# Optimization experiments

Measured on AMD Instinct MI355X. Metric: run time of the kernel, lower is better.

Reference implementation:

```python
import jax, jax.numpy as jnp
import numpy as np

B, T, ENC, DEC, U = 64, 2048, 512, 512, 128

def setup_inputs() -> dict:
    key = jax.random.key(0)
    ks = jax.random.split(key, 8)
    s_dec = 1.0 / np.sqrt(DEC)
    s_enc = 1.0 / np.sqrt(ENC)
    s_u = 1.0 / np.sqrt(U)
    return {
        "decoder_hidden": jax.random.normal(ks[0], (B, DEC), jnp.float32),
        "encoder_outputs": jax.random.normal(ks[1], (B, T, ENC), jnp.float32),
        "Wa": jax.random.normal(ks[2], (DEC, U), jnp.float32) * s_dec,
        "ba": jnp.zeros((U,), jnp.float32),
        "Wb": jax.random.normal(ks[3], (ENC, U), jnp.float32) * s_enc,
        "bb": jnp.zeros((U,), jnp.float32),
        "Wv": jax.random.normal(ks[4], (U, 1), jnp.float32) * s_u,
        "bv": jnp.zeros((1,), jnp.float32),
    }

def reference(decoder_hidden, encoder_outputs, Wa, ba, Wb, bb, Wv, bv):
    # q: [B, 1, U] — decoder hidden projected, broadcast over time
    q = (decoder_hidden @ Wa + ba)[:, None, :]
    # k: [B, T, U]
    k = jnp.einsum('bte,eu->btu', encoder_outputs, Wb) + bb
    # score: [B, T, 1]
    score = jnp.tanh(q + k) @ Wv + bv
    attn = jax.nn.softmax(score, axis=1)          # [B, T, 1]
    context = jnp.sum(attn * encoder_outputs, axis=1)  # [B, ENC]
    return context, attn
```

## Files before the change

kernel.cpp:

```cpp
#include <hip/hip_runtime.h>
#include <math.h>

#define B_   64
#define T_   2048
#define ENC_ 512
#define U_   128
#define NC   16
#define MBLK 128

typedef __attribute__((ext_vector_type(8))) _Float16 half8;
typedef __attribute__((ext_vector_type(4))) float float4v;

__device__ __forceinline__ void async_ld16(const void* g, void* l) {
    __builtin_amdgcn_global_load_lds(
        (const __attribute__((address_space(1))) void*)g,
        (__attribute__((address_space(3))) void*)l, 16, 0, 0);
}

__device__ inline void cvt_split8_f16(const float4 a0, const float4 a1,
                                      half8& h, half8& l) {
    const float xs[8] = {a0.x, a0.y, a0.z, a0.w, a1.x, a1.y, a1.z, a1.w};
#pragma unroll
    for (int j = 0; j < 8; ++j) {
        const _Float16 hi = (_Float16)xs[j];
        h[j] = hi;
        l[j] = (_Float16)(xs[j] - (float)hi);
    }
}

__device__ inline float fast_tanh(float x) {
    const float e = __expf(2.0f * x);
    return 1.0f - 2.0f / (e + 1.0f);
}

__global__ __launch_bounds__(256)
void prep_kernel(const float* __restrict__ dh,
                 const float* __restrict__ Wa,
                 const float* __restrict__ ba,
                 const float* __restrict__ bb,
                 const float* __restrict__ Wb,
                 float* __restrict__ q,
                 _Float16* __restrict__ whf,
                 float* __restrict__ uz) {
    const int blk = blockIdx.x;
    const int tid = threadIdx.x;
    if (blk < 64) {
        if (tid < U_) {
            const int b = blk, u = tid;
            const float* dhb = dh + b * ENC_;
            float a0 = 0.f, a1 = 0.f, a2 = 0.f, a3 = 0.f;
#pragma unroll 4
            for (int e = 0; e < ENC_; e += 4) {
                a0 += dhb[e + 0] * Wa[(e + 0) * U_ + u];
                a1 += dhb[e + 1] * Wa[(e + 1) * U_ + u];
                a2 += dhb[e + 2] * Wa[(e + 2) * U_ + u];
                a3 += dhb[e + 3] * Wa[(e + 3) * U_ + u];
            }
            q[b * U_ + u] = ((a0 + a1) + (a2 + a3)) + ba[u] + bb[u];
        }
    } else if (blk < 96) {
        const int fid = (blk - 64) * 4 + (tid >> 6);
        const int c   = fid >> 3;
        const int gn  = fid & 7;
        const int L   = tid & 63;
        const int n   = gn * 16 + (L & 15);
        const int k0  = c * 32 + (L >> 4) * 8;
        half8 hi;
#pragma unroll
        for (int j = 0; j < 8; ++j)
            hi[j] = (_Float16)Wb[(size_t)(k0 + j) * U_ + n];
        *(half8*)(whf + ((size_t)fid * 64 + L) * 8) = hi;
    } else {
        const int i = (blk - 96) * 256 + tid;
        if (i < B_ * ENC_ + B_) uz[i] = 0.f;
    }
}

__global__ __launch_bounds__(256, 3)
void score_ctx_kernel(const float* __restrict__ enc,
                      const _Float16* __restrict__ whf,
                      const float* __restrict__ q,
                      const float* __restrict__ Wv,
                      float* __restrict__ expw,
                      float* __restrict__ uctx,
                      float* __restrict__ Zsum) {
    __shared__ __align__(16) float    As[2][4096];
    __shared__ __align__(16) _Float16 Bs[2][4096];
    __shared__ float ew[MBLK];

    const int tid = threadIdx.x;
    const int w   = tid >> 6;
    const int L   = tid & 63;
    const int m0  = blockIdx.x * MBLK;
    const int b   = m0 >> 11;

    const int arow = w * 32 + (L >> 3);
    const int akf  = ((L & 7) ^ (L >> 3)) * 4;
    const float* aprow = enc + (size_t)(m0 + arow) * ENC_ + akf;
    const _Float16* bprow = whf + w * 1024 + L * 8;

    float4v acc[2][8];
#pragma unroll
    for (int mi = 0; mi < 2; ++mi)
#pragma unroll
        for (int gi = 0; gi < 8; ++gi) acc[mi][gi] = (float4v)0.f;

    {
#pragma unroll
        for (int j = 0; j < 4; ++j)
            async_ld16(aprow + (size_t)j * 8 * ENC_, &As[0][w * 1024 + j * 256]);
#pragma unroll
        for (int j = 0; j < 2; ++j)
            async_ld16(bprow + j * 512, &Bs[0][w * 1024 + j * 512]);
    }
    __syncthreads();

    for (int c = 0; c < NC; ++c) {
        const int cur = c & 1;

        if (c < NC - 1) {
            const int nxt = cur ^ 1;
            const float* ap = aprow + (c + 1) * 32;
#pragma unroll
            for (int j = 0; j < 4; ++j)
                async_ld16(ap + (size_t)j * 8 * ENC_, &As[nxt][w * 1024 + j * 256]);
            const _Float16* bp = bprow + (size_t)(c + 1) * 4096;
#pragma unroll
            for (int j = 0; j < 2; ++j)
                async_ld16(bp + j * 512, &Bs[nxt][w * 1024 + j * 512]);
        }

        half8 bh[8];
#pragma unroll
        for (int gi = 0; gi < 8; ++gi)
            bh[gi] = *(const half8*)(&Bs[cur][(gi * 64 + L) * 8]);

        half8 ah[2], al[2];
#pragma unroll
        for (int mi = 0; mi < 2; ++mi) {
            const int row = w * 32 + mi * 16 + (L & 15);
            const int s4  = (row & 7) * 4;
            const int k0  = (L >> 4) * 8;
            const float4 x0 = *(const float4*)(&As[cur][row * 32 + (k0 ^ s4)]);
            const float4 x1 = *(const float4*)(&As[cur][row * 32 + ((k0 + 4) ^ s4)]);
            cvt_split8_f16(x0, x1, ah[mi], al[mi]);
        }

#pragma unroll
        for (int mi = 0; mi < 2; ++mi)
#pragma unroll
            for (int gi = 0; gi < 8; ++gi) {
                acc[mi][gi] = __builtin_amdgcn_mfma_f32_16x16x32_f16(ah[mi], bh[gi], acc[mi][gi], 0, 0, 0);
                acc[mi][gi] = __builtin_amdgcn_mfma_f32_16x16x32_f16(al[mi], bh[gi], acc[mi][gi], 0, 0, 0);
            }

        __syncthreads();
    }

    const int n15 = L & 15;
    float qv[8], wvv[8];
#pragma unroll
    for (int gi = 0; gi < 8; ++gi) {
        const int u = gi * 16 + n15;
        qv[gi]  = q[b * U_ + u];
        wvv[gi] = Wv[u];
    }
#pragma unroll
    for (int mi = 0; mi < 2; ++mi) {
#pragma unroll
        for (int r = 0; r < 4; ++r) {
            float s = 0.f;
#pragma unroll
            for (int gi = 0; gi < 8; ++gi)
                s += fast_tanh(qv[gi] + acc[mi][gi][r]) * wvv[gi];
            s += __shfl_xor(s, 1, 64);
            s += __shfl_xor(s, 2, 64);
            s += __shfl_xor(s, 4, 64);
            s += __shfl_xor(s, 8, 64);
            if (n15 == 0) {
                const int mrow = w * 32 + mi * 16 + (L >> 4) * 4 + r;
                const float e = __expf(s);
                ew[mrow] = e;
                expw[m0 + mrow] = e;
            }
        }
    }
    __syncthreads();

    const int col = tid * 2;
    const float* ebase = enc + (size_t)m0 * ENC_ + col;
    float sx = 0.f, sy = 0.f;
#pragma unroll 8
    for (int t = 0; t < MBLK; ++t) {
        const float wgt = ew[t];
        const float2 v = *(const float2*)(ebase + (size_t)t * ENC_);
        sx += wgt * v.x;
        sy += wgt * v.y;
    }
    atomicAdd(&uctx[b * ENC_ + col], sx);
    atomicAdd(&uctx[b * ENC_ + col + 1], sy);

    if (tid < 64) {
        float z = ew[tid] + ew[tid + 64];
        z += __shfl_xor(z, 1, 64);
        z += __shfl_xor(z, 2, 64);
        z += __shfl_xor(z, 4, 64);
        z += __shfl_xor(z, 8, 64);
        z += __shfl_xor(z, 16, 64);
        z += __shfl_xor(z, 32, 64);
        if (tid == 0) atomicAdd(&Zsum[b], z);
    }
}

__global__ void normalize_kernel(const float* __restrict__ uctx,
                                 const float* __restrict__ Zsum,
                                 const float* __restrict__ expw,
                                 float* __restrict__ ctx,
                                 float* __restrict__ attn) {
    const int idx = blockIdx.x * 256 + threadIdx.x;
    if (idx < B_ * ENC_) {
        ctx[idx] = uctx[idx] / Zsum[idx >> 9];
    } else {
        const int i2 = idx - B_ * ENC_;
        attn[i2] = expw[i2] / Zsum[i2 >> 11];
    }
}

extern "C" void kernel_launch(void* const* d_in, const int* in_sizes, int n_in,
                              void* d_out, int out_size, void* d_ws, size_t ws_size,
                              hipStream_t stream) {
    const float* dh  = (const float*)d_in[0];
    const float* enc = (const float*)d_in[1];
    const float* Wa  = (const float*)d_in[2];
    const float* ba  = (const float*)d_in[3];
    const float* Wb  = (const float*)d_in[4];
    const float* bb  = (const float*)d_in[5];
    const float* Wv  = (const float*)d_in[6];

    float* out      = (float*)d_out;
    float* ctx      = out;
    float* attn_out = out + (B_ * ENC_);

    float* ws   = (float*)d_ws;
    float* q    = ws;
    float* expw = ws + 8192;
    float* uctx = ws + 8192 + B_ * T_;
    float* Zs   = uctx + B_ * ENC_;
    _Float16* whf = (_Float16*)(Zs + 64);

    prep_kernel<<<225, 256, 0, stream>>>(dh, Wa, ba, bb, Wb, q, whf, uctx);
    score_ctx_kernel<<<(B_ * T_) / MBLK, 256, 0, stream>>>(enc, whf, q, Wv,
                                                           expw, uctx, Zs);
    normalize_kernel<<<(B_ * (ENC_ + T_)) / 256, 256, 0, stream>>>(uctx, Zs, expw,
                                                                   ctx, attn_out);
}
```

Baseline: 437.8 us.

## Load Wb fragments directly to registers and replace block barriers with per-wave waitcnts

Wb fragments are now read straight from global memory into registers each chunk instead of being staged through LDS, which removes the Bs shared buffer. Each wave loads and consumes only its own rows of the A tile, so the per-iteration __syncthreads is replaced by manual s_waitcnt vmcnt/lgkmcnt counters, with the last chunk peeled out of the loop. The aim is to cut barrier stalls and LDS traffic and to lower LDS use per block. The risk is that the hand-set vmcnt values must exactly match the number of outstanding loads the compiler issues, and global B loads add L2 traffic and latency to every chunk.

```diff
diff --git a/kernel.cpp b/kernel.cpp
--- a/kernel.cpp
+++ b/kernel.cpp
@@ -84,8 +84,7 @@
                       float* __restrict__ expw,
                       float* __restrict__ uctx,
                       float* __restrict__ Zsum) {
-    __shared__ __align__(16) float    As[2][4096];
-    __shared__ __align__(16) _Float16 Bs[2][4096];
+    __shared__ __align__(16) float As[2][4096];
     __shared__ float ew[MBLK];
 
     const int tid = threadIdx.x;
@@ -97,7 +96,6 @@
     const int arow = w * 32 + (L >> 3);
     const int akf  = ((L & 7) ^ (L >> 3)) * 4;
     const float* aprow = enc + (size_t)(m0 + arow) * ENC_ + akf;
-    const _Float16* bprow = whf + w * 1024 + L * 8;
 
     float4v acc[2][8];
 #pragma unroll
@@ -105,35 +103,27 @@
 #pragma unroll
         for (int gi = 0; gi < 8; ++gi) acc[mi][gi] = (float4v)0.f;
 
-    {
+#pragma unroll
+    for (int j = 0; j < 4; ++j)
+        async_ld16(aprow + (size_t)j * 8 * ENC_, &As[0][w * 1024 + j * 256]);
+
+    for (int c = 0; c < NC - 1; ++c) {
+        const int cur = c & 1;
+        const int nxt = cur ^ 1;
+
+        half8 bh[8];
+        const _Float16* bp = whf + (size_t)c * 4096 + L * 8;
+#pragma unroll
+        for (int gi = 0; gi < 8; ++gi)
+            bh[gi] = *(const half8*)(bp + gi * 512);
+
+        asm volatile("s_waitcnt lgkmcnt(0)" ::: "memory");
+        const float* ap = aprow + (c + 1) * 32;
 #pragma unroll
         for (int j = 0; j < 4; ++j)
-            async_ld16(aprow + (size_t)j * 8 * ENC_, &As[0][w * 1024 + j * 256]);
-#pragma unroll
-        for (int j = 0; j < 2; ++j)
-            async_ld16(bprow + j * 512, &Bs[0][w * 1024 + j * 512]);
-    }
-    __syncthreads();
-
-    for (int c = 0; c < NC; ++c) {
-        const int cur = c & 1;
-
-        if (c < NC - 1) {
-            const int nxt = cur ^ 1;
-            const float* ap = aprow + (c + 1) * 32;
-#pragma unroll
-            for (int j = 0; j < 4; ++j)
-                async_ld16(ap + (size_t)j * 8 * ENC_, &As[nxt][w * 1024 + j * 256]);
-            const _Float16* bp = bprow + (size_t)(c + 1) * 4096;
-#pragma unroll
-            for (int j = 0; j < 2; ++j)
-                async_ld16(bp + j * 512, &Bs[nxt][w * 1024 + j * 512]);
-        }
-
-        half8 bh[8];
-#pragma unroll
-        for (int gi = 0; gi < 8; ++gi)
-            bh[gi] = *(const half8*)(&Bs[cur][(gi * 64 + L) * 8]);
+            async_ld16(ap + (size_t)j * 8 * ENC_, &As[nxt][w * 1024 + j * 256]);
+
+        asm volatile("s_waitcnt vmcnt(12)" ::: "memory");
 
         half8 ah[2], al[2];
 #pragma unroll
@@ -153,8 +143,36 @@
                 acc[mi][gi] = __builtin_amdgcn_mfma_f32_16x16x32_f16(ah[mi], bh[gi], acc[mi][gi], 0, 0, 0);
                 acc[mi][gi] = __builtin_amdgcn_mfma_f32_16x16x32_f16(al[mi], bh[gi], acc[mi][gi], 0, 0, 0);
             }
-
-        __syncthreads();
+    }
+
+    {
+        const int c   = NC - 1;
+        const int cur = c & 1;
+        half8 bh[8];
+        const _Float16* bp = whf + (size_t)c * 4096 + L * 8;
+#pragma unroll
+        for (int gi = 0; gi < 8; ++gi)
+            bh[gi] = *(const half8*)(bp + gi * 512);
+
+        asm volatile("s_waitcnt vmcnt(8)" ::: "memory");
+
+        half8 ah[2], al[2];
+#pragma unroll
+        for (int mi = 0; mi < 2; ++mi) {
+            const int row = w * 32 + mi * 16 + (L & 15);
+            const int s4  = (row & 7) * 4;
+            const int k0  = (L >> 4) * 8;
+            const float4 x0 = *(const float4*)(&As[cur][row * 32 + (k0 ^ s4)]);
+            const float4 x1 = *(const float4*)(&As[cur][row * 32 + ((k0 + 4) ^ s4)]);
+            cvt_split8_f16(x0, x1, ah[mi], al[mi]);
+        }
+#pragma unroll
+        for (int mi = 0; mi < 2; ++mi)
+#pragma unroll
+            for (int gi = 0; gi < 8; ++gi) {
+                acc[mi][gi] = __builtin_amdgcn_mfma_f32_16x16x32_f16(ah[mi], bh[gi], acc[mi][gi], 0, 0, 0);
+                acc[mi][gi] = __builtin_amdgcn_mfma_f32_16x16x32_f16(al[mi], bh[gi], acc[mi][gi], 0, 0, 0);
+            }
     }
 
     const int n15 = L & 15;
```

Result: no change. 431.1 us (-1.5%).

## Remove block barriers with per-wave 4-stage A pipeline and register-prefetched B

Applied to the files above, without the earlier changes.

Each wave now loads only its own A rows into a 4-deep LDS ring and waits with explicit vmcnt/lgkmcnt counts, so the per-chunk __syncthreads is dropped. The fp16 B fragments are prefetched straight from global memory into registers one chunk ahead instead of staged through shared memory. The LDS layout gains padding (GSTRIDE) and a new swizzle. This adds register pressure, so the occupancy hint drops from 3 to 2 blocks, and correctness depends on the hand-counted waitcnt values matching the issued loads.

```diff
diff --git a/kernel.cpp b/kernel.cpp
--- a/kernel.cpp
+++ b/kernel.cpp
@@ -7,6 +7,7 @@
 #define U_   128
 #define NC   16
 #define MBLK 128
+#define GSTRIDE 264
 
 typedef __attribute__((ext_vector_type(8))) _Float16 half8;
 typedef __attribute__((ext_vector_type(4))) float float4v;
@@ -76,7 +77,7 @@
     }
 }
 
-__global__ __launch_bounds__(256, 3)
+__global__ __launch_bounds__(256, 2)
 void score_ctx_kernel(const float* __restrict__ enc,
                       const _Float16* __restrict__ whf,
                       const float* __restrict__ q,
@@ -84,8 +85,7 @@
                       float* __restrict__ expw,
                       float* __restrict__ uctx,
                       float* __restrict__ Zsum) {
-    __shared__ __align__(16) float    As[2][4096];
-    __shared__ __align__(16) _Float16 Bs[2][4096];
+    __shared__ __align__(16) float As[4][16 * GSTRIDE];
     __shared__ float ew[MBLK];
 
     const int tid = threadIdx.x;
@@ -97,7 +97,6 @@
     const int arow = w * 32 + (L >> 3);
     const int akf  = ((L & 7) ^ (L >> 3)) * 4;
     const float* aprow = enc + (size_t)(m0 + arow) * ENC_ + akf;
-    const _Float16* bprow = whf + w * 1024 + L * 8;
 
     float4v acc[2][8];
 #pragma unroll
@@ -105,44 +104,53 @@
 #pragma unroll
         for (int gi = 0; gi < 8; ++gi) acc[mi][gi] = (float4v)0.f;
 
+#pragma unroll
+    for (int j = 0; j < 4; ++j)
+        async_ld16(aprow + (size_t)j * 8 * ENC_, &As[0][(w * 4 + j) * GSTRIDE]);
+#pragma unroll
+    for (int j = 0; j < 4; ++j)
+        async_ld16(aprow + 32 + (size_t)j * 8 * ENC_, &As[1][(w * 4 + j) * GSTRIDE]);
+    half8 pb[8];
     {
-#pragma unroll
-        for (int j = 0; j < 4; ++j)
-            async_ld16(aprow + (size_t)j * 8 * ENC_, &As[0][w * 1024 + j * 256]);
-#pragma unroll
-        for (int j = 0; j < 2; ++j)
-            async_ld16(bprow + j * 512, &Bs[0][w * 1024 + j * 512]);
-    }
-    __syncthreads();
-
+        const _Float16* bp = whf + L * 8;
+#pragma unroll
+        for (int gi = 0; gi < 8; ++gi) pb[gi] = *(const half8*)(bp + gi * 512);
+    }
+
+#pragma unroll
     for (int c = 0; c < NC; ++c) {
-        const int cur = c & 1;
-
-        if (c < NC - 1) {
-            const int nxt = cur ^ 1;
-            const float* ap = aprow + (c + 1) * 32;
+        half8 bh[8];
+#pragma unroll
+        for (int gi = 0; gi < 8; ++gi) bh[gi] = pb[gi];
+
+        if (c + 1 < NC) {
+            const _Float16* bp = whf + (size_t)(c + 1) * 4096 + L * 8;
+#pragma unroll
+            for (int gi = 0; gi < 8; ++gi) pb[gi] = *(const half8*)(bp + gi * 512);
+        }
+
+        if (c + 2 < NC) {
+            asm volatile("s_waitcnt lgkmcnt(0)" ::: "memory");
+            const float* ap = aprow + (c + 2) * 32;
 #pragma unroll
             for (int j = 0; j < 4; ++j)
-                async_ld16(ap + (size_t)j * 8 * ENC_, &As[nxt][w * 1024 + j * 256]);
-            const _Float16* bp = bprow + (size_t)(c + 1) * 4096;
-#pragma unroll
-            for (int j = 0; j < 2; ++j)
-                async_ld16(bp + j * 512, &Bs[nxt][w * 1024 + j * 512]);
-        }
-
-        half8 bh[8];
-#pragma unroll
-        for (int gi = 0; gi < 8; ++gi)
-            bh[gi] = *(const half8*)(&Bs[cur][(gi * 64 + L) * 8]);
-
+                async_ld16(ap + (size_t)j * 8 * ENC_,
+                           &As[(c + 2) & 3][(w * 4 + j) * GSTRIDE]);
+        }
+
+        if (c < NC - 2)       asm volatile("s_waitcnt vmcnt(24)" ::: "memory");
+        else if (c == NC - 2) asm volatile("s_waitcnt vmcnt(20)" ::: "memory");
+        else                  asm volatile("s_waitcnt vmcnt(8)"  ::: "memory");
+
+        const float* Ab = &As[c & 3][0];
         half8 ah[2], al[2];
 #pragma unroll
         for (int mi = 0; mi < 2; ++mi) {
-            const int row = w * 32 + mi * 16 + (L & 15);
-            const int s4  = (row & 7) * 4;
-            const int k0  = (L >> 4) * 8;
-            const float4 x0 = *(const float4*)(&As[cur][row * 32 + (k0 ^ s4)]);
-            const float4 x1 = *(const float4*)(&As[cur][row * 32 + ((k0 + 4) ^ s4)]);
+            const int g  = w * 4 + mi * 2 + ((L >> 3) & 1);
+            const int rr = L & 7;
+            const int kg = (L >> 4) * 2;
+            const float4 x0 = *(const float4*)(Ab + g * GSTRIDE + rr * 32 + ((kg ^ rr) * 4));
+            const float4 x1 = *(const float4*)(Ab + g * GSTRIDE + rr * 32 + (((kg + 1) ^ rr) * 4));
             cvt_split8_f16(x0, x1, ah[mi], al[mi]);
         }
 
@@ -153,8 +161,6 @@
                 acc[mi][gi] = __builtin_amdgcn_mfma_f32_16x16x32_f16(ah[mi], bh[gi], acc[mi][gi], 0, 0, 0);
                 acc[mi][gi] = __builtin_amdgcn_mfma_f32_16x16x32_f16(al[mi], bh[gi], acc[mi][gi], 0, 0, 0);
             }
-
-        __syncthreads();
     }
 
     const int n15 = L & 15;
```

New measurement: 427.5 us. 2.4% less time.

## Stage whole encoder tile as split-f16 in LDS and reuse it for context

Applied to the files above, without the earlier changes.

The block tile shrinks to 32 rows. The whole 32x512 encoder slab is loaded once, split into hi/lo f16 and stored in swizzled LDS. The Wb fragments now stream from global memory straight into registers through a 3-deep register prefetch, and four waves split the N dimension in two, with partial scores combined through shared memory. The context sum reads the LDS copy instead of reloading encoder rows from global memory, which removes the second global pass over the encoder. The cost is 4x more blocks and atomics, 64KB of LDS per block (occupancy hint lowered to 2), and a context computed from the hi+lo f16 reconstruction.

```diff
diff --git a/kernel.cpp b/kernel.cpp
--- a/kernel.cpp
+++ b/kernel.cpp
@@ -6,22 +6,16 @@
 #define ENC_ 512
 #define U_   128
 #define NC   16
-#define MBLK 128
+#define MBLK 32
 
 typedef __attribute__((ext_vector_type(8))) _Float16 half8;
+typedef __attribute__((ext_vector_type(4))) _Float16 half4;
 typedef __attribute__((ext_vector_type(4))) float float4v;
 
-__device__ __forceinline__ void async_ld16(const void* g, void* l) {
-    __builtin_amdgcn_global_load_lds(
-        (const __attribute__((address_space(1))) void*)g,
-        (__attribute__((address_space(3))) void*)l, 16, 0, 0);
-}
-
-__device__ inline void cvt_split8_f16(const float4 a0, const float4 a1,
-                                      half8& h, half8& l) {
-    const float xs[8] = {a0.x, a0.y, a0.z, a0.w, a1.x, a1.y, a1.z, a1.w};
-#pragma unroll
-    for (int j = 0; j < 8; ++j) {
+__device__ inline void cvt_split4(const float4 a, half4& h, half4& l) {
+    const float xs[4] = {a.x, a.y, a.z, a.w};
+#pragma unroll
+    for (int j = 0; j < 4; ++j) {
         const _Float16 hi = (_Float16)xs[j];
         h[j] = hi;
         l[j] = (_Float16)(xs[j] - (float)hi);
@@ -76,7 +70,7 @@
     }
 }
 
-__global__ __launch_bounds__(256, 3)
+__global__ __launch_bounds__(256, 2)
 void score_ctx_kernel(const float* __restrict__ enc,
                       const _Float16* __restrict__ whf,
                       const float* __restrict__ q,
@@ -84,8 +78,9 @@
                       float* __restrict__ expw,
                       float* __restrict__ uctx,
                       float* __restrict__ Zsum) {
-    __shared__ __align__(16) float    As[2][4096];
-    __shared__ __align__(16) _Float16 Bs[2][4096];
+    __shared__ __align__(16) _Float16 Ah[MBLK * ENC_];
+    __shared__ __align__(16) _Float16 Al[MBLK * ENC_];
+    __shared__ float sred[2 * MBLK];
     __shared__ float ew[MBLK];
 
     const int tid = threadIdx.x;
@@ -94,120 +89,128 @@
     const int m0  = blockIdx.x * MBLK;
     const int b   = m0 >> 11;
 
-    const int arow = w * 32 + (L >> 3);
-    const int akf  = ((L & 7) ^ (L >> 3)) * 4;
-    const float* aprow = enc + (size_t)(m0 + arow) * ENC_ + akf;
-    const _Float16* bprow = whf + w * 1024 + L * 8;
-
-    float4v acc[2][8];
-#pragma unroll
-    for (int mi = 0; mi < 2; ++mi)
-#pragma unroll
-        for (int gi = 0; gi < 8; ++gi) acc[mi][gi] = (float4v)0.f;
-
     {
-#pragma unroll
-        for (int j = 0; j < 4; ++j)
-            async_ld16(aprow + (size_t)j * 8 * ENC_, &As[0][w * 1024 + j * 256]);
-#pragma unroll
-        for (int j = 0; j < 2; ++j)
-            async_ld16(bprow + j * 512, &Bs[0][w * 1024 + j * 512]);
+        const int l = L;
+        const int g = w;
+        float4 xa[8], xb[8];
+#pragma unroll
+        for (int j = 0; j < 8; ++j) {
+            const float* rp = enc + (size_t)(m0 + j * 4 + g) * ENC_;
+            xa[j] = *(const float4*)(rp + l * 4);
+            xb[j] = *(const float4*)(rp + 256 + l * 4);
+        }
+#pragma unroll
+        for (int j = 0; j < 8; ++j) {
+            const int row = j * 4 + g;
+            const int rs  = row & 7;
+            const int rb  = row * ENC_;
+            {
+                half4 h, lo; cvt_split4(xa[j], h, lo);
+                const int off = rb + (((l >> 1) ^ rs) * 8) + (l & 1) * 4;
+                *(half4*)(Ah + off) = h;  *(half4*)(Al + off) = lo;
+            }
+            {
+                half4 h, lo; cvt_split4(xb[j], h, lo);
+                const int off = rb + ((((l >> 1) + 32) ^ rs) * 8) + (l & 1) * 4;
+                *(half4*)(Ah + off) = h;  *(half4*)(Al + off) = lo;
+            }
+        }
     }
     __syncthreads();
 
+    const int wr  = w >> 1;
+    const int wc  = w & 1;
+    const int n15 = L & 15;
+    const int aq  = L >> 4;
+    const int arow  = wr * 16 + n15;
+    const int abase = arow * ENC_;
+    const int ars   = arow & 7;
+
+    float4v acc[4];
+#pragma unroll
+    for (int gi = 0; gi < 4; ++gi) acc[gi] = (float4v)0.f;
+
+    half8 pb[3][4];
+#pragma unroll
+    for (int gi = 0; gi < 4; ++gi) {
+        pb[0][gi] = *(const half8*)(whf + ((size_t)((0 * 8 + wc * 4 + gi) * 64 + L)) * 8);
+        pb[1][gi] = *(const half8*)(whf + ((size_t)((1 * 8 + wc * 4 + gi) * 64 + L)) * 8);
+    }
+
+#pragma unroll
     for (int c = 0; c < NC; ++c) {
-        const int cur = c & 1;
-
-        if (c < NC - 1) {
-            const int nxt = cur ^ 1;
-            const float* ap = aprow + (c + 1) * 32;
-#pragma unroll
-            for (int j = 0; j < 4; ++j)
-                async_ld16(ap + (size_t)j * 8 * ENC_, &As[nxt][w * 1024 + j * 256]);
-            const _Float16* bp = bprow + (size_t)(c + 1) * 4096;
-#pragma unroll
-            for (int j = 0; j < 2; ++j)
-                async_ld16(bp + j * 512, &Bs[nxt][w * 1024 + j * 512]);
-        }
-
-        half8 bh[8];
-#pragma unroll
-        for (int gi = 0; gi < 8; ++gi)
-            bh[gi] = *(const half8*)(&Bs[cur][(gi * 64 + L) * 8]);
-
-        half8 ah[2], al[2];
-#pragma unroll
-        for (int mi = 0; mi < 2; ++mi) {
-            const int row = w * 32 + mi * 16 + (L & 15);
-            const int s4  = (row & 7) * 4;
-            const int k0  = (L >> 4) * 8;
-            const float4 x0 = *(const float4*)(&As[cur][row * 32 + (k0 ^ s4)]);
-            const float4 x1 = *(const float4*)(&As[cur][row * 32 + ((k0 + 4) ^ s4)]);
-            cvt_split8_f16(x0, x1, ah[mi], al[mi]);
-        }
-
-#pragma unroll
-        for (int mi = 0; mi < 2; ++mi)
-#pragma unroll
-            for (int gi = 0; gi < 8; ++gi) {
-                acc[mi][gi] = __builtin_amdgcn_mfma_f32_16x16x32_f16(ah[mi], bh[gi], acc[mi][gi], 0, 0, 0);
-                acc[mi][gi] = __builtin_amdgcn_mfma_f32_16x16x32_f16(al[mi], bh[gi], acc[mi][gi], 0, 0, 0);
-            }
-
-        __syncthreads();
-    }
-
-    const int n15 = L & 15;
-    float qv[8], wvv[8];
-#pragma unroll
-    for (int gi = 0; gi < 8; ++gi) {
-        const int u = gi * 16 + n15;
+        if (c + 2 < NC) {
+#pragma unroll
+            for (int gi = 0; gi < 4; ++gi)
+                pb[(c + 2) % 3][gi] = *(const half8*)(whf +
+                    ((size_t)(((c + 2) * 8 + wc * 4 + gi) * 64 + L)) * 8);
+        }
+        const int slot = (c * 4 + aq) ^ ars;
+        const half8 ah = *(const half8*)(Ah + abase + slot * 8);
+        const half8 al = *(const half8*)(Al + abase + slot * 8);
+#pragma unroll
+        for (int gi = 0; gi < 4; ++gi) {
+            acc[gi] = __builtin_amdgcn_mfma_f32_16x16x32_f16(ah, pb[c % 3][gi], acc[gi], 0, 0, 0);
+            acc[gi] = __builtin_amdgcn_mfma_f32_16x16x32_f16(al, pb[c % 3][gi], acc[gi], 0, 0, 0);
+        }
+    }
+
+    float qv[4], wvv[4];
+#pragma unroll
+    for (int gi = 0; gi < 4; ++gi) {
+        const int u = wc * 64 + gi * 16 + n15;
         qv[gi]  = q[b * U_ + u];
         wvv[gi] = Wv[u];
     }
 #pragma unroll
-    for (int mi = 0; mi < 2; ++mi) {
-#pragma unroll
-        for (int r = 0; r < 4; ++r) {
-            float s = 0.f;
-#pragma unroll
-            for (int gi = 0; gi < 8; ++gi)
-                s += fast_tanh(qv[gi] + acc[mi][gi][r]) * wvv[gi];
-            s += __shfl_xor(s, 1, 64);
-            s += __shfl_xor(s, 2, 64);
-            s += __shfl_xor(s, 4, 64);
-            s += __shfl_xor(s, 8, 64);
-            if (n15 == 0) {
-                const int mrow = w * 32 + mi * 16 + (L >> 4) * 4 + r;
-                const float e = __expf(s);
-                ew[mrow] = e;
-                expw[m0 + mrow] = e;
-            }
+    for (int r = 0; r < 4; ++r) {
+        float s = 0.f;
+#pragma unroll
+        for (int gi = 0; gi < 4; ++gi)
+            s += fast_tanh(qv[gi] + acc[gi][r]) * wvv[gi];
+        s += __shfl_xor(s, 1, 64);
+        s += __shfl_xor(s, 2, 64);
+        s += __shfl_xor(s, 4, 64);
+        s += __shfl_xor(s, 8, 64);
+        if (n15 == 0) {
+            const int brow = wr * 16 + (L >> 4) * 4 + r;
+            sred[wc * MBLK + brow] = s;
         }
     }
     __syncthreads();
 
-    const int col = tid * 2;
-    const float* ebase = enc + (size_t)m0 * ENC_ + col;
+    if (tid < MBLK) {
+        const float s = sred[tid] + sred[MBLK + tid];
+        const float e = __expf(s);
+        ew[tid] = e;
+        expw[m0 + tid] = e;
+    }
+    __syncthreads();
+
+    typedef __attribute__((ext_vector_type(2))) _Float16 half2v;
+    const int p2oct = tid >> 2;
+    const int p2in  = (tid & 3) * 2;
     float sx = 0.f, sy = 0.f;
 #pragma unroll 8
-    for (int t = 0; t < MBLK; ++t) {
-        const float wgt = ew[t];
-        const float2 v = *(const float2*)(ebase + (size_t)t * ENC_);
-        sx += wgt * v.x;
-        sy += wgt * v.y;
-    }
+    for (int r = 0; r < MBLK; ++r) {
+        const int off = r * ENC_ + ((p2oct ^ (r & 7)) * 8) + p2in;
+        const half2v h = *(const half2v*)(Ah + off);
+        const half2v lo = *(const half2v*)(Al + off);
+        const float wgt = ew[r];
+        sx += wgt * ((float)h[0] + (float)lo[0]);
+        sy += wgt * ((float)h[1] + (float)lo[1]);
+    }
+    const int col = tid * 2;
     atomicAdd(&uctx[b * ENC_ + col], sx);
     atomicAdd(&uctx[b * ENC_ + col + 1], sy);
 
-    if (tid < 64) {
-        float z = ew[tid] + ew[tid + 64];
+    if (tid < MBLK) {
+        float z = ew[tid];
         z += __shfl_xor(z, 1, 64);
         z += __shfl_xor(z, 2, 64);
         z += __shfl_xor(z, 4, 64);
         z += __shfl_xor(z, 8, 64);
         z += __shfl_xor(z, 16, 64);
-        z += __shfl_xor(z, 32, 64);
         if (tid == 0) atomicAdd(&Zsum[b], z);
     }
 }
```

After: 452.8 us. +3.4%, slower.
